# Kernel tuning notes

Hardware: AMD Instinct MI355X
Metric: run time of the kernel (lower is better)

## Reference

```python
import jax, jax.numpy as jnp
import numpy as np

B, D, T = 16, 2048, 100
N0, N1, N2 = 4096, 4096, 2048
THRESH, DECAY, REFRAC = 1.0, 0.9, 2
LR, TRACE_DECAY = 0.01, 0.95
NUM_CLASSES = 10


def setup_inputs() -> dict:
    key = jax.random.key(0)
    k = jax.random.split(key, 8)
    x = jax.random.normal(k[0], (B, D), dtype=jnp.float32)
    u = jax.random.uniform(k[1], (B, T, N0), dtype=jnp.float32)
    W_enc = jax.random.normal(k[2], (D, N0), dtype=jnp.float32) * 0.02
    b_enc = jnp.zeros((N0,), jnp.float32)
    W0 = jax.random.normal(k[3], (N0, N1), dtype=jnp.float32) * 0.1
    W1 = jax.random.normal(k[4], (N1, N2), dtype=jnp.float32) * 0.1
    W_dec = jax.random.normal(k[5], (N2, NUM_CLASSES), dtype=jnp.float32) * 0.02
    b_dec = jnp.zeros((NUM_CLASSES,), jnp.float32)
    return {"x": x, "u": u, "W_enc": W_enc, "b_enc": b_enc,
            "W0": W0, "W1": W1, "W_dec": W_dec, "b_dec": b_dec}


def _lif(V, refr, current):
    """Leaky integrate-and-fire: V <- decay*V + I; spike if V>thr and not refractory."""
    V = DECAY * V + current
    spk = (V > THRESH) & (refr <= 0)
    V = jnp.where(spk, 0.0, V)
    refr = jnp.where(spk, REFRAC, jnp.maximum(refr - 1, 0))
    return V, refr, spk.astype(current.dtype)


def _forward(x, u, W_enc, b_enc, W0, W1, W_dec, b_dec):
    # Rate-coded spike encoding: Bernoulli(sigmoid(Wx+b)) via the supplied uniform noise u.
    rates = jax.nn.sigmoid(x @ W_enc + b_enc)               # (B, N0)
    spikes_in = (u < rates[:, None, :]).astype(x.dtype)      # (B, T, N0)

    def step(carry, s_in):
        V0, V1, V2, r0, r1, r2, p0, q0, p1, q1, Wa, Wb = carry
        # layer-wise LIF dynamics
        V0, r0, s0 = _lif(V0, r0, s_in)
        V1, r1, s1 = _lif(V1, r1, s0 @ Wa)
        V2, r2, s2 = _lif(V2, r2, s1 @ Wb)
        # STDP synapse 0 (N0 -> N1): exponential traces + outer-product update, clamp to [-1, 1]
        p0 = TRACE_DECAY * p0 + s0
        q0 = TRACE_DECAY * q0 + s1
        dWa = LR * (jnp.einsum('bi,bj->ij', p0, s1) - jnp.einsum('bi,bj->ij', s0, q0))
        Wa = jnp.clip(Wa + dWa, -1.0, 1.0)
        # STDP synapse 1 (N1 -> N2)
        p1 = TRACE_DECAY * p1 + s1
        q1 = TRACE_DECAY * q1 + s2
        dWb = LR * (jnp.einsum('bi,bj->ij', p1, s2) - jnp.einsum('bi,bj->ij', s1, q1))
        Wb = jnp.clip(Wb + dWb, -1.0, 1.0)
        return (V0, V1, V2, r0, r1, r2, p0, q0, p1, q1, Wa, Wb), s2

    f = x.dtype
    carry0 = (jnp.zeros((B, N0), f), jnp.zeros((B, N1), f), jnp.zeros((B, N2), f),
              jnp.zeros((B, N0), jnp.int32), jnp.zeros((B, N1), jnp.int32), jnp.zeros((B, N2), jnp.int32),
              jnp.zeros((B, N0), f), jnp.zeros((B, N1), f),
              jnp.zeros((B, N1), f), jnp.zeros((B, N2), f),
              W0, W1)
    _, s2_seq = jax.lax.scan(step, carry0, jnp.swapaxes(spikes_in, 0, 1))  # (T, B, N2)
    spike_counts = s2_seq.sum(axis=0)                        # (B, N2)
    return spike_counts @ W_dec + b_dec                      # (B, 10)


def reference(x, u, W_enc, b_enc, W0, W1, W_dec, b_dec):
    return _forward(x, u, W_enc, b_enc, W0, W1, W_dec, b_dec)
```

## Files before the change

### kernel.cpp

```cpp
#include <hip/hip_runtime.h>
#include <math.h>

#define B_  16
#define D_  2048
#define T_  100
#define N0_ 4096
#define N1_ 4096
#define N2_ 2048
#define NC_ 10

__global__ __launch_bounds__(256) void rates_kernel(
    const float* __restrict__ x, const float* __restrict__ W_enc,
    const float* __restrict__ b_enc, float* __restrict__ rates)
{
    int tid = blockIdx.x * 256 + threadIdx.x;
    int b = tid >> 12, i = tid & (N0_ - 1);
    const float* xr = x + b * D_;
    float acc = 0.f;
    for (int d = 0; d < D_; ++d)
        acc = fmaf(xr[d], W_enc[(size_t)d * N0_ + i], acc);
    float z = __fadd_rn(acc, b_enc[i]);
    rates[tid] = 1.0f / (1.0f + expf(-z));
}

__global__ __launch_bounds__(256) void layer0_kernel(
    const float* __restrict__ u, const float* __restrict__ rates,
    float* __restrict__ s0_all, float* __restrict__ p0_all)
{
    int tid = blockIdx.x * 256 + threadIdx.x;
    int b = tid & (B_ - 1), i = tid >> 4;
    float rate = rates[b * N0_ + i];
    const float* ub = u + (size_t)b * T_ * N0_ + i;
    float V = 0.f, refr = 0.f, p0 = 0.f;
    for (int t = 0; t < T_; ++t) {
        float uv = ub[(size_t)t * N0_];
        float s_in = (uv < rate) ? 1.0f : 0.0f;
        V = __fadd_rn(__fmul_rn(0.9f, V), s_in);
        bool spk = (V > 1.0f) && (refr <= 0.0f);
        float s = spk ? 1.0f : 0.0f;
        V = spk ? 0.0f : V;
        refr = spk ? 2.0f : fmaxf(refr - 1.0f, 0.0f);
        p0 = __fadd_rn(__fmul_rn(0.95f, p0), s);
        size_t idx = ((size_t)t * N0_ + i) * B_ + b;
        s0_all[idx] = s;
        p0_all[idx] = p0;
    }
}

__device__ __forceinline__ float dot16(const float4 r[4], const float* v) {
    float t = 0.f;
    t = fmaf(r[0].x, v[0], t);  t = fmaf(r[0].y, v[1], t);
    t = fmaf(r[0].z, v[2], t);  t = fmaf(r[0].w, v[3], t);
    t = fmaf(r[1].x, v[4], t);  t = fmaf(r[1].y, v[5], t);
    t = fmaf(r[1].z, v[6], t);  t = fmaf(r[1].w, v[7], t);
    t = fmaf(r[2].x, v[8], t);  t = fmaf(r[2].y, v[9], t);
    t = fmaf(r[2].z, v[10], t); t = fmaf(r[2].w, v[11], t);
    t = fmaf(r[3].x, v[12], t); t = fmaf(r[3].y, v[13], t);
    t = fmaf(r[3].z, v[14], t); t = fmaf(r[3].w, v[15], t);
    return t;
}
__device__ __forceinline__ void acc16(float* acc, const float4 r[4], float w) {
    acc[0]  = fmaf(r[0].x, w, acc[0]);  acc[1]  = fmaf(r[0].y, w, acc[1]);
    acc[2]  = fmaf(r[0].z, w, acc[2]);  acc[3]  = fmaf(r[0].w, w, acc[3]);
    acc[4]  = fmaf(r[1].x, w, acc[4]);  acc[5]  = fmaf(r[1].y, w, acc[5]);
    acc[6]  = fmaf(r[1].z, w, acc[6]);  acc[7]  = fmaf(r[1].w, w, acc[7]);
    acc[8]  = fmaf(r[2].x, w, acc[8]);  acc[9]  = fmaf(r[2].y, w, acc[9]);
    acc[10] = fmaf(r[2].z, w, acc[10]); acc[11] = fmaf(r[2].w, w, acc[11]);
    acc[12] = fmaf(r[3].x, w, acc[12]); acc[13] = fmaf(r[3].y, w, acc[13]);
    acc[14] = fmaf(r[3].z, w, acc[14]); acc[15] = fmaf(r[3].w, w, acc[15]);
}
__device__ __forceinline__ void ld_row4(float4 r[4], const float* p) {
    const float4* p4 = (const float4*)p;
    r[0] = p4[0]; r[1] = p4[1]; r[2] = p4[2]; r[3] = p4[3];
}

__global__ __launch_bounds__(256, 4) void ka_kernel(
    float* __restrict__ Wa,
    const float* __restrict__ s0_all,
    const float* __restrict__ p0_all,
    const float* __restrict__ s1_bj,
    const float* __restrict__ q0_bj,
    float* __restrict__ pa, int t, int store_w)
{
    const int jt = blockIdx.x >> 6;
    const int chunk = blockIdx.x & 63;
    const int j0 = jt * 256 + threadIdx.x;
    const int i0 = chunk * 64;
    const int prev = 1 - (t & 1);

    float acc0[B_];
    #pragma unroll
    for (int b = 0; b < B_; ++b) acc0[b] = 0.f;

    const float* s0t = s0_all + (size_t)t * N0_ * B_;

    if (t > 0) {
        float s1v0[B_], q0v0[B_];
        #pragma unroll
        for (int b = 0; b < B_; ++b) {
            s1v0[b] = s1_bj[((size_t)prev * B_ + b) * N1_ + j0];
            q0v0[b] = q0_bj[((size_t)prev * B_ + b) * N1_ + j0];
        }
        const float* s0p = s0_all + (size_t)(t - 1) * N0_ * B_;
        const float* p0p = p0_all + (size_t)(t - 1) * N0_ * B_;
        float w0 = Wa[(size_t)i0 * N1_ + j0];
        #pragma unroll 2
        for (int ii = 0; ii < 64; ++ii) {
            const int i = i0 + ii;
            const int ip = (ii < 63) ? (i + 1) : i;
            float w0n = Wa[(size_t)ip * N1_ + j0];
            float4 p0r[4], s0r[4], s0tr[4];
            ld_row4(p0r,  p0p + (size_t)i * B_);
            ld_row4(s0r,  s0p + (size_t)i * B_);
            ld_row4(s0tr, s0t + (size_t)i * B_);
            float t1a = dot16(p0r, s1v0), t2a = dot16(s0r, q0v0);
            float wn0 = __fadd_rn(w0, __fmul_rn(0.01f, __fsub_rn(t1a, t2a)));
            wn0 = fminf(fmaxf(wn0, -1.0f), 1.0f);
            if (store_w)
                Wa[(size_t)i * N1_ + j0] = wn0;
            acc16(acc0, s0tr, wn0);
            w0 = w0n;
        }
    } else {
        #pragma unroll 2
        for (int ii = 0; ii < 64; ++ii) {
            const int i = i0 + ii;
            float4 s0tr[4];
            ld_row4(s0tr, s0t + (size_t)i * B_);
            float w0 = Wa[(size_t)i * N1_ + j0];
            acc16(acc0, s0tr, w0);
        }
    }
    #pragma unroll
    for (int b = 0; b < B_; ++b)
        pa[((size_t)chunk * B_ + b) * N1_ + j0] = acc0[b];
}

__global__ __launch_bounds__(256) void lif1_kernel(
    const float* __restrict__ pa, float* __restrict__ V1, float* __restrict__ r1,
    float* __restrict__ s1_bj, float* __restrict__ s1_jb,
    float* __restrict__ q0_bj, float* __restrict__ p1_jb, int t)
{
    int tid = blockIdx.x * 256 + threadIdx.x;
    int b = tid >> 12, j = tid & (N1_ - 1);
    float y = 0.f;
    #pragma unroll 16
    for (int c = 0; c < 64; ++c) y += pa[((size_t)c * B_ + b) * N1_ + j];
    float V = __fadd_rn(__fmul_rn(0.9f, V1[tid]), y);
    float rr = r1[tid];
    bool spk = (V > 1.0f) && (rr <= 0.0f);
    float s = spk ? 1.0f : 0.0f;
    V1[tid] = spk ? 0.0f : V;
    r1[tid] = spk ? 2.0f : fmaxf(rr - 1.0f, 0.0f);
    int cur = t & 1, prev = 1 - cur;
    s1_bj[(size_t)cur * B_ * N1_ + tid] = s;
    s1_jb[(size_t)cur * B_ * N1_ + (size_t)j * B_ + b] = s;
    float q0 = __fadd_rn(__fmul_rn(0.95f, q0_bj[(size_t)prev * B_ * N1_ + tid]), s);
    q0_bj[(size_t)cur * B_ * N1_ + tid] = q0;
    float p1 = __fadd_rn(__fmul_rn(0.95f, p1_jb[(size_t)prev * B_ * N1_ + (size_t)j * B_ + b]), s);
    p1_jb[(size_t)cur * B_ * N1_ + (size_t)j * B_ + b] = p1;
}

__global__ __launch_bounds__(256, 4) void kb_kernel(
    float* __restrict__ Wb,
    const float* __restrict__ s1_jb,
    const float* __restrict__ p1_jb,
    const float* __restrict__ s2_bk,
    const float* __restrict__ q1_bk,
    float* __restrict__ pb, int t, int store_w)
{
    const int kt = blockIdx.x >> 7;
    const int chunk = blockIdx.x & 127;
    const int k0 = kt * 256 + threadIdx.x;
    const int j0 = chunk * 32;
    const int cur = t & 1, prev = 1 - cur;

    float acc0[B_];
    #pragma unroll
    for (int b = 0; b < B_; ++b) acc0[b] = 0.f;

    const float* s1c = s1_jb + (size_t)cur * N1_ * B_;

    if (t > 0) {
        float s2v0[B_], q1v0[B_];
        #pragma unroll
        for (int b = 0; b < B_; ++b) {
            s2v0[b] = s2_bk[((size_t)prev * B_ + b) * N2_ + k0];
            q1v0[b] = q1_bk[((size_t)prev * B_ + b) * N2_ + k0];
        }
        const float* p1p = p1_jb + (size_t)prev * N1_ * B_;
        const float* s1p = s1_jb + (size_t)prev * N1_ * B_;
        float w0 = Wb[(size_t)j0 * N2_ + k0];
        #pragma unroll 2
        for (int jj = j0; jj < j0 + 32; ++jj) {
            const int jp = (jj < j0 + 31) ? (jj + 1) : jj;
            float w0n = Wb[(size_t)jp * N2_ + k0];
            float4 p1r[4], s1pr[4], s1cr[4];
            ld_row4(p1r,  p1p + (size_t)jj * B_);
            ld_row4(s1pr, s1p + (size_t)jj * B_);
            ld_row4(s1cr, s1c + (size_t)jj * B_);
            float t1a = dot16(p1r, s2v0), t2a = dot16(s1pr, q1v0);
            float wn0 = __fadd_rn(w0, __fmul_rn(0.01f, __fsub_rn(t1a, t2a)));
            wn0 = fminf(fmaxf(wn0, -1.0f), 1.0f);
            if (store_w)
                Wb[(size_t)jj * N2_ + k0] = wn0;
            acc16(acc0, s1cr, wn0);
            w0 = w0n;
        }
    } else {
        #pragma unroll 2
        for (int jj = j0; jj < j0 + 32; ++jj) {
            float4 s1cr[4];
            ld_row4(s1cr, s1c + (size_t)jj * B_);
            float w0 = Wb[(size_t)jj * N2_ + k0];
            acc16(acc0, s1cr, w0);
        }
    }
    #pragma unroll
    for (int b = 0; b < B_; ++b)
        pb[((size_t)chunk * B_ + b) * N2_ + k0] = acc0[b];
}

__global__ __launch_bounds__(256) void lif2_kernel(
    const float* __restrict__ pb, float* __restrict__ V2, float* __restrict__ r2,
    float* __restrict__ s2_bk, float* __restrict__ q1_bk,
    float* __restrict__ counts, int t)
{
    int tid = blockIdx.x * 256 + threadIdx.x;
    int b = tid >> 11, k = tid & (N2_ - 1);
    float y = 0.f;
    #pragma unroll 16
    for (int c = 0; c < 128; ++c) y += pb[((size_t)c * B_ + b) * N2_ + k];
    float V = __fadd_rn(__fmul_rn(0.9f, V2[tid]), y);
    float rr = r2[tid];
    bool spk = (V > 1.0f) && (rr <= 0.0f);
    float s = spk ? 1.0f : 0.0f;
    V2[tid] = spk ? 0.0f : V;
    r2[tid] = spk ? 2.0f : fmaxf(rr - 1.0f, 0.0f);
    int cur = t & 1, prev = 1 - cur;
    s2_bk[(size_t)cur * B_ * N2_ + tid] = s;
    float q1 = __fadd_rn(__fmul_rn(0.95f, q1_bk[(size_t)prev * B_ * N2_ + tid]), s);
    q1_bk[(size_t)cur * B_ * N2_ + tid] = q1;
    counts[tid] = counts[tid] + s;
}

__global__ __launch_bounds__(256) void decode_kernel(
    const float* __restrict__ counts, const float* __restrict__ W_dec,
    const float* __restrict__ b_dec, float* __restrict__ out)
{
    int tid = threadIdx.x;
    if (tid < B_ * NC_) {
        int b = tid / NC_, c = tid % NC_;
        float a = 0.f;
        for (int k = 0; k < N2_; ++k)
            a = fmaf(counts[(size_t)b * N2_ + k], W_dec[(size_t)k * NC_ + c], a);
        out[tid] = __fadd_rn(a, b_dec[c]);
    }
}

extern "C" void kernel_launch(void* const* d_in, const int* in_sizes, int n_in,
                              void* d_out, int out_size, void* d_ws, size_t ws_size,
                              hipStream_t stream) {
    const float* x     = (const float*)d_in[0];
    const float* u     = (const float*)d_in[1];
    const float* W_enc = (const float*)d_in[2];
    const float* b_enc = (const float*)d_in[3];
    float* Wa          = (float*)d_in[4];
    float* Wb          = (float*)d_in[5];
    const float* W_dec = (const float*)d_in[6];
    const float* b_dec = (const float*)d_in[7];
    float* out         = (float*)d_out;

    float* ws = (float*)d_ws;
    size_t off = 0;
    float* rates  = ws + off; off += (size_t)B_ * N0_;
    float* s0_all = ws + off; off += (size_t)T_ * N0_ * B_;
    float* p0_all = ws + off; off += (size_t)T_ * N0_ * B_;
    float* s1_bj  = ws + off; off += 2 * (size_t)B_ * N1_;
    float* s1_jb  = ws + off; off += 2 * (size_t)B_ * N1_;
    float* pa     = ws + off; off += 64 * (size_t)B_ * N1_;
    float* pb     = ws + off; off += 128 * (size_t)B_ * N2_;
    float* zblock = ws + off;
    float* q0_bj  = ws + off; off += 2 * (size_t)B_ * N1_;
    float* p1_jb  = ws + off; off += 2 * (size_t)B_ * N1_;
    float* q1_bk  = ws + off; off += 2 * (size_t)B_ * N2_;
    float* s2_bk  = ws + off; off += 2 * (size_t)B_ * N2_;
    float* V1     = ws + off; off += (size_t)B_ * N1_;
    float* r1     = ws + off; off += (size_t)B_ * N1_;
    float* V2     = ws + off; off += (size_t)B_ * N2_;
    float* r2     = ws + off; off += (size_t)B_ * N2_;
    float* counts = ws + off; off += (size_t)B_ * N2_;
    size_t zbytes = (size_t)((ws + off) - zblock) * sizeof(float);

    hipMemsetAsync(zblock, 0, zbytes, stream);
    rates_kernel<<<256, 256, 0, stream>>>(x, W_enc, b_enc, rates);
    layer0_kernel<<<256, 256, 0, stream>>>(u, rates, s0_all, p0_all);
    for (int t = 0; t < T_; ++t) {
        int store_w = (t < T_ - 1) ? 1 : 0;
        ka_kernel<<<1024, 256, 0, stream>>>(Wa, s0_all, p0_all, s1_bj, q0_bj, pa, t, store_w);
        lif1_kernel<<<256, 256, 0, stream>>>(pa, V1, r1, s1_bj, s1_jb, q0_bj, p1_jb, t);
        kb_kernel<<<1024, 256, 0, stream>>>(Wb, s1_jb, p1_jb, s2_bk, q1_bk, pb, t, store_w);
        lif2_kernel<<<128, 256, 0, stream>>>(pb, V2, r2, s2_bk, q1_bk, counts, t);
    }
    decode_kernel<<<1, 256, 0, stream>>>(counts, W_dec, b_dec, out);
}
```

Baseline: 7.493 ms.

## Fuse layer-2 LIF of previous step into next step's Wa STDP kernel

The layer-2 LIF update for step t-1 now runs as 128 extra blocks appended to the step-t Wa kernel launch instead of as its own kernel, and one trailing lif2 launch handles the final step. Each step needs one fewer launch, and the small LIF work overlaps with the Wa update, which does not depend on it. In exchange, the lif2 result for step t-1 is produced later in the schedule. This is only correct if kb at step t reads s2_bk and q1_bk from the previous parity, before they would have been ready in the old schedule, so there is a risk around double-buffer indexing.

```diff
diff --git a/kernel.cpp b/kernel.cpp
--- a/kernel.cpp
+++ b/kernel.cpp
@@ -74,14 +74,41 @@
     r[0] = p4[0]; r[1] = p4[1]; r[2] = p4[2]; r[3] = p4[3];
 }
 
-__global__ __launch_bounds__(256, 4) void ka_kernel(
+__global__ __launch_bounds__(256, 4) void ka_lif2_kernel(
     float* __restrict__ Wa,
     const float* __restrict__ s0_all,
     const float* __restrict__ p0_all,
     const float* __restrict__ s1_bj,
     const float* __restrict__ q0_bj,
-    float* __restrict__ pa, int t, int store_w)
-{
+    float* __restrict__ pa,
+    const float* __restrict__ pb,
+    float* __restrict__ V2, float* __restrict__ r2,
+    float* __restrict__ s2_bk, float* __restrict__ q1_bk,
+    float* __restrict__ counts,
+    int t, int store_w)
+{
+    if (blockIdx.x >= 1024) {
+        if (t == 0) return;
+        const int tm1 = t - 1;
+        int tid = (blockIdx.x - 1024) * 256 + threadIdx.x;
+        int b = tid >> 11, k = tid & (N2_ - 1);
+        float y = 0.f;
+        #pragma unroll 16
+        for (int c = 0; c < 128; ++c) y += pb[((size_t)c * B_ + b) * N2_ + k];
+        float V = __fadd_rn(__fmul_rn(0.9f, V2[tid]), y);
+        float rr = r2[tid];
+        bool spk = (V > 1.0f) && (rr <= 0.0f);
+        float s = spk ? 1.0f : 0.0f;
+        V2[tid] = spk ? 0.0f : V;
+        r2[tid] = spk ? 2.0f : fmaxf(rr - 1.0f, 0.0f);
+        int cur = tm1 & 1, prev = 1 - cur;
+        s2_bk[(size_t)cur * B_ * N2_ + tid] = s;
+        float q1 = __fadd_rn(__fmul_rn(0.95f, q1_bk[(size_t)prev * B_ * N2_ + tid]), s);
+        q1_bk[(size_t)cur * B_ * N2_ + tid] = q1;
+        counts[tid] = counts[tid] + s;
+        return;
+    }
+
     const int jt = blockIdx.x >> 6;
     const int chunk = blockIdx.x & 63;
     const int j0 = jt * 256 + threadIdx.x;
@@ -297,10 +324,12 @@
     layer0_kernel<<<256, 256, 0, stream>>>(u, rates, s0_all, p0_all);
     for (int t = 0; t < T_; ++t) {
         int store_w = (t < T_ - 1) ? 1 : 0;
-        ka_kernel<<<1024, 256, 0, stream>>>(Wa, s0_all, p0_all, s1_bj, q0_bj, pa, t, store_w);
+        ka_lif2_kernel<<<1152, 256, 0, stream>>>(Wa, s0_all, p0_all, s1_bj, q0_bj, pa,
+                                                 pb, V2, r2, s2_bk, q1_bk, counts,
+                                                 t, store_w);
         lif1_kernel<<<256, 256, 0, stream>>>(pa, V1, r1, s1_bj, s1_jb, q0_bj, p1_jb, t);
         kb_kernel<<<1024, 256, 0, stream>>>(Wb, s1_jb, p1_jb, s2_bk, q1_bk, pb, t, store_w);
-        lif2_kernel<<<128, 256, 0, stream>>>(pb, V2, r2, s2_bk, q1_bk, counts, t);
-    }
+    }
+    lif2_kernel<<<128, 256, 0, stream>>>(pb, V2, r2, s2_bk, q1_bk, counts, T_ - 1);
     decode_kernel<<<1, 256, 0, stream>>>(counts, W_dec, b_dec, out);
 }
```

New measurement: 6.980 ms. 1.07x faster.

## Software-pipeline layer-2 STDP matmul of step t-1 with layer-1 of step t

Applied to the files above, without the earlier changes.

Merges the two matmul+STDP kernels into one launch, where blocks 0-1023 handle layer 1 at step t and blocks 1024-2047 handle layer 2 at step t-1. The two LIF kernels are merged the same way, and the loop runs T+1 times. This halves the number of kernel launches and the launch and drain gaps. It also gives each launch more independent blocks, so the two layers' work can overlap on the GPU. The cost is an extra pipeline step and reliance on double-buffer parity to keep read and write hazards apart within the stream order.

```diff
diff --git a/kernel.cpp b/kernel.cpp
--- a/kernel.cpp
+++ b/kernel.cpp
@@ -74,106 +74,88 @@
     r[0] = p4[0]; r[1] = p4[1]; r[2] = p4[2]; r[3] = p4[3];
 }
 
-__global__ __launch_bounds__(256, 4) void ka_kernel(
+__global__ __launch_bounds__(256, 4) void step_mm_kernel(
     float* __restrict__ Wa,
     const float* __restrict__ s0_all,
     const float* __restrict__ p0_all,
     const float* __restrict__ s1_bj,
     const float* __restrict__ q0_bj,
-    float* __restrict__ pa, int t, int store_w)
-{
-    const int jt = blockIdx.x >> 6;
-    const int chunk = blockIdx.x & 63;
-    const int j0 = jt * 256 + threadIdx.x;
-    const int i0 = chunk * 64;
-    const int prev = 1 - (t & 1);
-
-    float acc0[B_];
-    #pragma unroll
-    for (int b = 0; b < B_; ++b) acc0[b] = 0.f;
-
-    const float* s0t = s0_all + (size_t)t * N0_ * B_;
-
-    if (t > 0) {
-        float s1v0[B_], q0v0[B_];
-        #pragma unroll
-        for (int b = 0; b < B_; ++b) {
-            s1v0[b] = s1_bj[((size_t)prev * B_ + b) * N1_ + j0];
-            q0v0[b] = q0_bj[((size_t)prev * B_ + b) * N1_ + j0];
-        }
-        const float* s0p = s0_all + (size_t)(t - 1) * N0_ * B_;
-        const float* p0p = p0_all + (size_t)(t - 1) * N0_ * B_;
-        float w0 = Wa[(size_t)i0 * N1_ + j0];
-        #pragma unroll 2
-        for (int ii = 0; ii < 64; ++ii) {
-            const int i = i0 + ii;
-            const int ip = (ii < 63) ? (i + 1) : i;
-            float w0n = Wa[(size_t)ip * N1_ + j0];
-            float4 p0r[4], s0r[4], s0tr[4];
-            ld_row4(p0r,  p0p + (size_t)i * B_);
-            ld_row4(s0r,  s0p + (size_t)i * B_);
-            ld_row4(s0tr, s0t + (size_t)i * B_);
-            float t1a = dot16(p0r, s1v0), t2a = dot16(s0r, q0v0);
-            float wn0 = __fadd_rn(w0, __fmul_rn(0.01f, __fsub_rn(t1a, t2a)));
-            wn0 = fminf(fmaxf(wn0, -1.0f), 1.0f);
-            if (store_w)
-                Wa[(size_t)i * N1_ + j0] = wn0;
-            acc16(acc0, s0tr, wn0);
-            w0 = w0n;
-        }
-    } else {
-        #pragma unroll 2
-        for (int ii = 0; ii < 64; ++ii) {
-            const int i = i0 + ii;
-            float4 s0tr[4];
-            ld_row4(s0tr, s0t + (size_t)i * B_);
-            float w0 = Wa[(size_t)i * N1_ + j0];
-            acc16(acc0, s0tr, w0);
-        }
-    }
-    #pragma unroll
-    for (int b = 0; b < B_; ++b)
-        pa[((size_t)chunk * B_ + b) * N1_ + j0] = acc0[b];
-}
-
-__global__ __launch_bounds__(256) void lif1_kernel(
-    const float* __restrict__ pa, float* __restrict__ V1, float* __restrict__ r1,
-    float* __restrict__ s1_bj, float* __restrict__ s1_jb,
-    float* __restrict__ q0_bj, float* __restrict__ p1_jb, int t)
-{
-    int tid = blockIdx.x * 256 + threadIdx.x;
-    int b = tid >> 12, j = tid & (N1_ - 1);
-    float y = 0.f;
-    #pragma unroll 16
-    for (int c = 0; c < 64; ++c) y += pa[((size_t)c * B_ + b) * N1_ + j];
-    float V = __fadd_rn(__fmul_rn(0.9f, V1[tid]), y);
-    float rr = r1[tid];
-    bool spk = (V > 1.0f) && (rr <= 0.0f);
-    float s = spk ? 1.0f : 0.0f;
-    V1[tid] = spk ? 0.0f : V;
-    r1[tid] = spk ? 2.0f : fmaxf(rr - 1.0f, 0.0f);
-    int cur = t & 1, prev = 1 - cur;
-    s1_bj[(size_t)cur * B_ * N1_ + tid] = s;
-    s1_jb[(size_t)cur * B_ * N1_ + (size_t)j * B_ + b] = s;
-    float q0 = __fadd_rn(__fmul_rn(0.95f, q0_bj[(size_t)prev * B_ * N1_ + tid]), s);
-    q0_bj[(size_t)cur * B_ * N1_ + tid] = q0;
-    float p1 = __fadd_rn(__fmul_rn(0.95f, p1_jb[(size_t)prev * B_ * N1_ + (size_t)j * B_ + b]), s);
-    p1_jb[(size_t)cur * B_ * N1_ + (size_t)j * B_ + b] = p1;
-}
-
-__global__ __launch_bounds__(256, 4) void kb_kernel(
+    float* __restrict__ pa,
     float* __restrict__ Wb,
     const float* __restrict__ s1_jb,
     const float* __restrict__ p1_jb,
     const float* __restrict__ s2_bk,
     const float* __restrict__ q1_bk,
-    float* __restrict__ pb, int t, int store_w)
-{
-    const int kt = blockIdx.x >> 7;
-    const int chunk = blockIdx.x & 127;
+    float* __restrict__ pb,
+    int t)
+{
+    if (blockIdx.x < 1024) {
+        if (t >= T_) return;
+        const int store_w = (t < T_ - 1) ? 1 : 0;
+        const int jt = blockIdx.x >> 6;
+        const int chunk = blockIdx.x & 63;
+        const int j0 = jt * 256 + threadIdx.x;
+        const int i0 = chunk * 64;
+        const int prev = 1 - (t & 1);
+
+        float acc0[B_];
+        #pragma unroll
+        for (int b = 0; b < B_; ++b) acc0[b] = 0.f;
+
+        const float* s0t = s0_all + (size_t)t * N0_ * B_;
+
+        if (t > 0) {
+            float s1v0[B_], q0v0[B_];
+            #pragma unroll
+            for (int b = 0; b < B_; ++b) {
+                s1v0[b] = s1_bj[((size_t)prev * B_ + b) * N1_ + j0];
+                q0v0[b] = q0_bj[((size_t)prev * B_ + b) * N1_ + j0];
+            }
+            const float* s0p = s0_all + (size_t)(t - 1) * N0_ * B_;
+            const float* p0p = p0_all + (size_t)(t - 1) * N0_ * B_;
+            float w0 = Wa[(size_t)i0 * N1_ + j0];
+            #pragma unroll 2
+            for (int ii = 0; ii < 64; ++ii) {
+                const int i = i0 + ii;
+                const int ip = (ii < 63) ? (i + 1) : i;
+                float w0n = Wa[(size_t)ip * N1_ + j0];
+                float4 p0r[4], s0r[4], s0tr[4];
+                ld_row4(p0r,  p0p + (size_t)i * B_);
+                ld_row4(s0r,  s0p + (size_t)i * B_);
+                ld_row4(s0tr, s0t + (size_t)i * B_);
+                float t1a = dot16(p0r, s1v0), t2a = dot16(s0r, q0v0);
+                float wn0 = __fadd_rn(w0, __fmul_rn(0.01f, __fsub_rn(t1a, t2a)));
+                wn0 = fminf(fmaxf(wn0, -1.0f), 1.0f);
+                if (store_w)
+                    Wa[(size_t)i * N1_ + j0] = wn0;
+                acc16(acc0, s0tr, wn0);
+                w0 = w0n;
+            }
+        } else {
+            #pragma unroll 2
+            for (int ii = 0; ii < 64; ++ii) {
+                const int i = i0 + ii;
+                float4 s0tr[4];
+                ld_row4(s0tr, s0t + (size_t)i * B_);
+                float w0 = Wa[(size_t)i * N1_ + j0];
+                acc16(acc0, s0tr, w0);
+            }
+        }
+        #pragma unroll
+        for (int b = 0; b < B_; ++b)
+            pa[((size_t)chunk * B_ + b) * N1_ + j0] = acc0[b];
+        return;
+    }
+
+    if (t == 0) return;
+    const int tb = t - 1;
+    const int store_w = (tb < T_ - 1) ? 1 : 0;
+    const int bx = blockIdx.x - 1024;
+    const int kt = bx >> 7;
+    const int chunk = bx & 127;
     const int k0 = kt * 256 + threadIdx.x;
     const int j0 = chunk * 32;
-    const int cur = t & 1, prev = 1 - cur;
+    const int cur = tb & 1, prev = 1 - cur;
 
     float acc0[B_];
     #pragma unroll
@@ -181,7 +163,7 @@
 
     const float* s1c = s1_jb + (size_t)cur * N1_ * B_;
 
-    if (t > 0) {
+    if (tb > 0) {
         float s2v0[B_], q1v0[B_];
         #pragma unroll
         for (int b = 0; b < B_; ++b) {
@@ -221,12 +203,41 @@
         pb[((size_t)chunk * B_ + b) * N2_ + k0] = acc0[b];
 }
 
-__global__ __launch_bounds__(256) void lif2_kernel(
+__global__ __launch_bounds__(256) void step_lif_kernel(
+    const float* __restrict__ pa, float* __restrict__ V1, float* __restrict__ r1,
+    float* __restrict__ s1_bj, float* __restrict__ s1_jb,
+    float* __restrict__ q0_bj, float* __restrict__ p1_jb,
     const float* __restrict__ pb, float* __restrict__ V2, float* __restrict__ r2,
     float* __restrict__ s2_bk, float* __restrict__ q1_bk,
-    float* __restrict__ counts, int t)
-{
-    int tid = blockIdx.x * 256 + threadIdx.x;
+    float* __restrict__ counts,
+    int t)
+{
+    if (blockIdx.x < 256) {
+        if (t >= T_) return;
+        int tid = blockIdx.x * 256 + threadIdx.x;
+        int b = tid >> 12, j = tid & (N1_ - 1);
+        float y = 0.f;
+        #pragma unroll 16
+        for (int c = 0; c < 64; ++c) y += pa[((size_t)c * B_ + b) * N1_ + j];
+        float V = __fadd_rn(__fmul_rn(0.9f, V1[tid]), y);
+        float rr = r1[tid];
+        bool spk = (V > 1.0f) && (rr <= 0.0f);
+        float s = spk ? 1.0f : 0.0f;
+        V1[tid] = spk ? 0.0f : V;
+        r1[tid] = spk ? 2.0f : fmaxf(rr - 1.0f, 0.0f);
+        int cur = t & 1, prev = 1 - cur;
+        s1_bj[(size_t)cur * B_ * N1_ + tid] = s;
+        s1_jb[(size_t)cur * B_ * N1_ + (size_t)j * B_ + b] = s;
+        float q0 = __fadd_rn(__fmul_rn(0.95f, q0_bj[(size_t)prev * B_ * N1_ + tid]), s);
+        q0_bj[(size_t)cur * B_ * N1_ + tid] = q0;
+        float p1 = __fadd_rn(__fmul_rn(0.95f, p1_jb[(size_t)prev * B_ * N1_ + (size_t)j * B_ + b]), s);
+        p1_jb[(size_t)cur * B_ * N1_ + (size_t)j * B_ + b] = p1;
+        return;
+    }
+
+    if (t == 0) return;
+    const int tb = t - 1;
+    int tid = (blockIdx.x - 256) * 256 + threadIdx.x;
     int b = tid >> 11, k = tid & (N2_ - 1);
     float y = 0.f;
     #pragma unroll 16
@@ -237,7 +248,7 @@
     float s = spk ? 1.0f : 0.0f;
     V2[tid] = spk ? 0.0f : V;
     r2[tid] = spk ? 2.0f : fmaxf(rr - 1.0f, 0.0f);
-    int cur = t & 1, prev = 1 - cur;
+    int cur = tb & 1, prev = 1 - cur;
     s2_bk[(size_t)cur * B_ * N2_ + tid] = s;
     float q1 = __fadd_rn(__fmul_rn(0.95f, q1_bk[(size_t)prev * B_ * N2_ + tid]), s);
     q1_bk[(size_t)cur * B_ * N2_ + tid] = q1;
@@ -295,12 +306,11 @@
     hipMemsetAsync(zblock, 0, zbytes, stream);
     rates_kernel<<<256, 256, 0, stream>>>(x, W_enc, b_enc, rates);
     layer0_kernel<<<256, 256, 0, stream>>>(u, rates, s0_all, p0_all);
-    for (int t = 0; t < T_; ++t) {
-        int store_w = (t < T_ - 1) ? 1 : 0;
-        ka_kernel<<<1024, 256, 0, stream>>>(Wa, s0_all, p0_all, s1_bj, q0_bj, pa, t, store_w);
-        lif1_kernel<<<256, 256, 0, stream>>>(pa, V1, r1, s1_bj, s1_jb, q0_bj, p1_jb, t);
-        kb_kernel<<<1024, 256, 0, stream>>>(Wb, s1_jb, p1_jb, s2_bk, q1_bk, pb, t, store_w);
-        lif2_kernel<<<128, 256, 0, stream>>>(pb, V2, r2, s2_bk, q1_bk, counts, t);
+    for (int t = 0; t <= T_; ++t) {
+        step_mm_kernel<<<2048, 256, 0, stream>>>(Wa, s0_all, p0_all, s1_bj, q0_bj, pa,
+                                                 Wb, s1_jb, p1_jb, s2_bk, q1_bk, pb, t);
+        step_lif_kernel<<<384, 256, 0, stream>>>(pa, V1, r1, s1_bj, s1_jb, q0_bj, p1_jb,
+                                                 pb, V2, r2, s2_bk, q1_bk, counts, t);
     }
     decode_kernel<<<1, 256, 0, stream>>>(counts, W_dec, b_dec, out);
 }
```

Measured after the change: 6.261 ms. 1.2x faster.
